# Optimization experiments

Measured on AMD Instinct MI355X. Metric: run time of the kernel, lower is better.

Reference implementation:

```python
import jax, jax.numpy as jnp
import numpy as np

NUM_HEADS = 32
HEAD_DIM = 128
HIDDEN = NUM_HEADS * HEAD_DIM  # 4096
ROPE_BASE = 10000.0
VISION_TOKEN_TYPE = 1


def vision_expert_mask(token_type_ids):
    # vision_token_mask[:, :-1] = (tt[:, :-1]==1) & (tt[:, 1:]==1); last col False
    tt = token_type_ids
    m = (tt[:, :-1] == VISION_TOKEN_TYPE) & (tt[:, 1:] == VISION_TOKEN_TYPE)
    return jnp.concatenate([m, jnp.zeros((tt.shape[0], 1), dtype=bool)], axis=1)


def rotary_cos_sin(position_ids, head_dim, dtype):
    inv_freq = 1.0 / (ROPE_BASE ** (jnp.arange(0, head_dim, 2, dtype=jnp.float32) / head_dim))
    freqs = position_ids.astype(jnp.float32)[..., None] * inv_freq  # [B,S,Dh/2]
    emb = jnp.concatenate([freqs, freqs], axis=-1)  # [B,S,Dh]
    return jnp.cos(emb).astype(dtype), jnp.sin(emb).astype(dtype)


def rotate_half(x):
    d = x.shape[-1] // 2
    return jnp.concatenate([-x[..., d:], x[..., :d]], axis=-1)


def setup_inputs() -> dict:
    key = jax.random.key(0)
    ks = jax.random.split(key, 5)
    B, S = 2, 2048
    hidden_states = jax.random.normal(ks[0], (B, S, HIDDEN), dtype=jnp.float32)
    token_type_ids = jax.random.randint(ks[1], (B, S), 0, 2, dtype=jnp.int64)
    position_ids = jnp.broadcast_to(jnp.arange(S, dtype=jnp.int64)[None, :], (B, S))
    scale = 0.02
    w_vis_qkv = jax.random.normal(ks[2], (HIDDEN, 3 * HIDDEN), dtype=jnp.float32) * scale
    w_lang_qkv = jax.random.normal(ks[3], (HIDDEN, 3 * HIDDEN), dtype=jnp.float32) * scale
    w_vis_dense = jax.random.normal(ks[4], (HIDDEN, HIDDEN), dtype=jnp.float32) * scale
    w_lang_dense = jax.random.normal(jax.random.fold_in(key, 7), (HIDDEN, HIDDEN), dtype=jnp.float32) * scale
    return dict(hidden_states=hidden_states, token_type_ids=token_type_ids,
                position_ids=position_ids, w_vis_qkv=w_vis_qkv, w_lang_qkv=w_lang_qkv,
                w_vis_dense=w_vis_dense, w_lang_dense=w_lang_dense)


def reference(hidden_states, token_type_ids, position_ids,
              w_vis_qkv, w_lang_qkv, w_vis_dense, w_lang_dense):
    B, S, D = hidden_states.shape
    vm = vision_expert_mask(token_type_ids)  # [B,S] bool

    # 2-expert QKV dispatch (mask-select between the two expert GEMMs)
    qkv = jnp.where(vm[..., None],
                    hidden_states @ w_vis_qkv,
                    hidden_states @ w_lang_qkv)  # [B,S,3D]
    q, k, v = jnp.split(qkv, 3, axis=-1)
    q = q.reshape(B, S, NUM_HEADS, HEAD_DIM)
    k = k.reshape(B, S, NUM_HEADS, HEAD_DIM)
    v = v.reshape(B, S, NUM_HEADS, HEAD_DIM)

    # rotary embedding on q, k
    cos, sin = rotary_cos_sin(position_ids, HEAD_DIM, q.dtype)  # [B,S,Dh]
    cos, sin = cos[:, :, None, :], sin[:, :, None, :]
    q = q * cos + rotate_half(q) * sin
    k = k * cos + rotate_half(k) * sin

    # causal attention (dense equivalent of the paged-attention call)
    scores = jnp.einsum('bqhd,bkhd->bhqk', q, k) / jnp.sqrt(jnp.array(HEAD_DIM, q.dtype))
    causal = jnp.tril(jnp.ones((S, S), dtype=bool))
    scores = jnp.where(causal[None, None], scores, jnp.finfo(scores.dtype).min)
    probs = jax.nn.softmax(scores, axis=-1)
    ctx = jnp.einsum('bhqk,bkhd->bqhd', probs, v).reshape(B, S, D)

    # 2-expert output dense dispatch
    attn_output = jnp.where(vm[..., None],
                            ctx @ w_vis_dense,
                            ctx @ w_lang_dense)
    return attn_output
```

## Files before the change

kernel.cpp:

```cpp
#include <hip/hip_runtime.h>
#include <math.h>

#define SEQ     2048
#define NB      2
#define NHEADS  32
#define DHEAD   128
#define HID     4096
#define NQKV    12288
#define T_TOKENS (NB*SEQ)

typedef _Float16 half8 __attribute__((ext_vector_type(8)));
typedef float v4f __attribute__((ext_vector_type(4)));

__device__ __forceinline__ void gload_lds16(const void* g, void* l) {
    __builtin_amdgcn_global_load_lds(
        (__attribute__((address_space(1))) void*)(void*)(g),
        (__attribute__((address_space(3))) void*)(unsigned)(unsigned long long)(l),
        16, 0, 0);
}

__device__ __forceinline__ v4f mfma16(half8 a, half8 b, v4f c) {
    return __builtin_amdgcn_mfma_f32_16x16x32_f16(a, b, c, 0, 0, 0);
}

__global__ void route_kernel(const int* __restrict__ tt, int* counts, int* idx) {
    int t = blockIdx.x * blockDim.x + threadIdx.x;
    if (t >= T_TOKENS) return;
    int s = t & (SEQ - 1);
    bool vm = (s < SEQ - 1) && (tt[t] == 1) && (tt[t + 1] == 1);
    int e = vm ? 0 : 1;
    int p = atomicAdd(&counts[e], 1);
    idx[e * T_TOKENS + p] = t;
}

__global__ void rope_table_kernel(const int* __restrict__ pos_ids, float2* __restrict__ tab) {
    int i = blockIdx.x * blockDim.x + threadIdx.x;
    if (i >= T_TOKENS * 64) return;
    int tok = i >> 6, j = i & 63;
    float invf = (float)pow(10000.0, -(double)j * (1.0 / 64.0));
    float ang = (float)pos_ids[tok] * invf;
    double ds, dc;
    sincos((double)ang, &ds, &dc);
    tab[i] = make_float2((float)dc, (float)ds);
}

__global__ void cvt_f32_f16(const float* __restrict__ src, _Float16* __restrict__ dst, int n4) {
    int i = blockIdx.x * blockDim.x + threadIdx.x;
    if (i >= n4) return;
    float4 v = ((const float4*)src)[i];
    union { _Float16 h[4]; uint2 u; } p;
    p.h[0] = (_Float16)v.x; p.h[1] = (_Float16)v.y;
    p.h[2] = (_Float16)v.z; p.h[3] = (_Float16)v.w;
    ((uint2*)dst)[i] = p.u;
}

__global__ void transpose_cvt(const float* __restrict__ W, _Float16* __restrict__ WT,
                              int K, int N) {
    __shared__ _Float16 t[64][72];
    const int n0 = blockIdx.x * 64, k0 = blockIdx.y * 64;
    const int cr = threadIdx.x & 15, rr = threadIdx.x >> 4;
#pragma unroll
    for (int it = 0; it < 4; ++it) {
        int r = rr + it * 16;
        float4 v = *(const float4*)&W[(size_t)(k0 + r) * N + n0 + cr * 4];
        t[cr*4+0][r] = (_Float16)v.x; t[cr*4+1][r] = (_Float16)v.y;
        t[cr*4+2][r] = (_Float16)v.z; t[cr*4+3][r] = (_Float16)v.w;
    }
    __syncthreads();
#pragma unroll
    for (int it = 0; it < 4; ++it) {
        int r = rr + it * 16;
        union { _Float16 h[4]; uint2 u; } p;
#pragma unroll
        for (int j = 0; j < 4; ++j) p.h[j] = t[r][cr*4+j];
        *(uint2*)&WT[(size_t)(n0 + r) * K + k0 + cr * 4] = p.u;
    }
}

__global__ void transpose_v(const _Float16* __restrict__ vin, _Float16* __restrict__ vout) {
    __shared__ _Float16 t[64][72];
    const int s0 = blockIdx.x * 64;
    const int d0 = blockIdx.y * 64;
    const int bh = blockIdx.z;
    const int b = bh >> 5, h = bh & 31;
    const int cr = threadIdx.x & 15, rr = threadIdx.x >> 4;
#pragma unroll
    for (int it = 0; it < 4; ++it) {
        int sl = rr + it * 16;
        union { _Float16 h4[4]; uint2 u; } p;
        p.u = *(const uint2*)&vin[(size_t)(b * SEQ + s0 + sl) * HID + h * DHEAD + d0 + cr * 4];
#pragma unroll
        for (int j = 0; j < 4; ++j) t[cr*4+j][sl] = p.h4[j];
    }
    __syncthreads();
#pragma unroll
    for (int it = 0; it < 4; ++it) {
        int dl = rr + it * 16;
        union { _Float16 h4[4]; uint2 u; } p;
#pragma unroll
        for (int j = 0; j < 4; ++j) p.h4[j] = t[dl][cr*4+j];
        *(uint2*)&vout[((size_t)bh * DHEAD + d0 + dl) * SEQ + s0 + cr * 4] = p.u;
    }
}

template <int MODE, int NCT>
__global__ __launch_bounds__(256, 2)
void gemm_expert(const _Float16* __restrict__ A,
                 const _Float16* __restrict__ BT0,
                 const _Float16* __restrict__ BT1,
                 const int* __restrict__ counts,
                 const int* __restrict__ idx_all,
                 const float2* __restrict__ rope,
                 _Float16* __restrict__ qbuf,
                 _Float16* __restrict__ kbuf,
                 _Float16* __restrict__ vbuf,
                 float* __restrict__ out) {
    const int e = blockIdx.z;
    const int count = counts[e];

    const int f   = blockIdx.x + NCT * blockIdx.y;
    const int xcd = f & 7;
    const int g   = f >> 3;
    const int c   = g >> 6;
    const int wi  = g & 63;
    const int rt  = wi >> 1;
    const int ct  = xcd * (NCT / 8) + c * 2 + (wi & 1);

    if (rt * 128 >= count) return;
    const int* idx = idx_all + e * T_TOKENS;
    const _Float16* BT = e ? BT1 : BT0;

    __shared__ _Float16 sA[4][128 * 32];
    __shared__ _Float16 sB[4][128 * 32];

    const int tid = threadIdx.x;
    const int w = tid >> 6, lane = tid & 63;
    const int col = lane & 15, quad = lane >> 4;

    const int r0 = (w * 2 + 0) * 16 + (lane >> 2);
    const int r1 = (w * 2 + 1) * 16 + (lane >> 2);
    int g0 = rt * 128 + r0; if (g0 > count - 1) g0 = count - 1;
    int g1 = rt * 128 + r1; if (g1 > count - 1) g1 = count - 1;
    const int tok0 = idx[g0], tok1 = idx[g1];
    const int schk = (lane & 3) ^ ((lane >> 3) & 3);
    const _Float16* ag0 = A + (size_t)tok0 * HID + schk * 8;
    const _Float16* ag1 = A + (size_t)tok1 * HID + schk * 8;
    const _Float16* bg0 = BT + (size_t)(ct * 128 + r0) * HID + schk * 8;
    const _Float16* bg1 = BT + (size_t)(ct * 128 + r1) * HID + schk * 8;
    const int sa_off0 = (w * 2 + 0) * 512;
    const int sa_off1 = (w * 2 + 1) * 512;

    v4f acc[2][8];
#pragma unroll
    for (int i = 0; i < 2; ++i)
#pragma unroll
        for (int j = 0; j < 8; ++j) { v4f z = {0.f, 0.f, 0.f, 0.f}; acc[i][j] = z; }

    const int kofq = (quad ^ ((col >> 1) & 3)) * 8;
    const int am0 = (w * 32 + col) * 32 + kofq;
    const int am1 = am0 + 16 * 32;

    auto stage = [&](int buf) {
        gload_lds16(ag0, &sA[buf][sa_off0]); gload_lds16(ag1, &sA[buf][sa_off1]);
        gload_lds16(bg0, &sB[buf][sa_off0]); gload_lds16(bg1, &sB[buf][sa_off1]);
        ag0 += 32; ag1 += 32; bg0 += 32; bg1 += 32;
    };
    auto compute = [&](int cur) {
        half8 a0 = *(const half8*)&sA[cur][am0];
        half8 a1 = *(const half8*)&sA[cur][am1];
#pragma unroll
        for (int nt = 0; nt < 8; ++nt) {
            half8 b = *(const half8*)&sB[cur][(nt * 16 + col) * 32 + kofq];
            acc[0][nt] = mfma16(a0, b, acc[0][nt]);
            acc[1][nt] = mfma16(a1, b, acc[1][nt]);
        }
    };

    const int NK = HID / 32;
    stage(0); stage(1); stage(2);

    for (int kt = 0; kt < NK - 3; ++kt) {
        asm volatile("s_waitcnt vmcnt(8)" ::: "memory");
        __builtin_amdgcn_s_barrier();
        asm volatile("" ::: "memory");
        stage((kt + 3) & 3);
        compute(kt & 3);
    }
    asm volatile("s_waitcnt vmcnt(8)" ::: "memory");
    __builtin_amdgcn_s_barrier();
    asm volatile("" ::: "memory");
    compute((NK - 3) & 3);
    asm volatile("s_waitcnt vmcnt(4)" ::: "memory");
    __builtin_amdgcn_s_barrier();
    asm volatile("" ::: "memory");
    compute((NK - 2) & 3);
    asm volatile("s_waitcnt vmcnt(0)" ::: "memory");
    __builtin_amdgcn_s_barrier();
    asm volatile("" ::: "memory");
    compute((NK - 1) & 3);

    const int n0 = ct * 128;
    if (MODE == 1) {
#pragma unroll
        for (int mt = 0; mt < 2; ++mt)
#pragma unroll
            for (int r = 0; r < 4; ++r) {
                int rg = rt * 128 + w * 32 + mt * 16 + quad * 4 + r;
                if (rg >= count) continue;
                int tok = idx[rg];
                float* dst = out + (size_t)tok * HID + n0;
#pragma unroll
                for (int nt = 0; nt < 8; ++nt) dst[nt * 16 + col] = acc[mt][nt][r];
            }
    } else {
        const int sec = n0 >> 12;
        const int h = (n0 >> 7) & 31;
#pragma unroll
        for (int mt = 0; mt < 2; ++mt)
#pragma unroll
            for (int r = 0; r < 4; ++r) {
                int rg = rt * 128 + w * 32 + mt * 16 + quad * 4 + r;
                if (rg >= count) continue;
                int tok = idx[rg];
                int b = tok >> 11, s = tok & (SEQ - 1);
                if (sec == 2) {
                    _Float16* dst = vbuf + (size_t)tok * HID + h * DHEAD;
#pragma unroll
                    for (int nt = 0; nt < 8; ++nt) dst[nt * 16 + col] = (_Float16)acc[mt][nt][r];
                } else {
                    _Float16* dst = (sec ? kbuf : qbuf) + ((size_t)(b * NHEADS + h) * SEQ + s) * DHEAD;
                    const float2* tp = rope + (size_t)tok * 64;
#pragma unroll
                    for (int nt = 0; nt < 4; ++nt) {
                        int d = nt * 16 + col;
                        float2 cs = tp[d];
                        float x = acc[mt][nt][r], y = acc[mt][nt + 4][r];
                        dst[d]      = (_Float16)(x * cs.x - y * cs.y);
                        dst[d + 64] = (_Float16)(y * cs.x + x * cs.y);
                    }
                }
            }
    }
}

__global__ __launch_bounds__(256, 2)
void attn_kernel(const _Float16* __restrict__ qbuf,
                 const _Float16* __restrict__ kbuf,
                 const _Float16* __restrict__ vt,
                 _Float16* __restrict__ ctx) {
    const int f   = blockIdx.x;
    const int xcd = f & 7;
    const int t   = f >> 3;
    const int s   = t & 31;
    const int rr  = t >> 5;
    const int u   = s & 15, g = s >> 4;
    const int bh  = xcd * 8 + rr * 2 + g;
    const int qt  = (rr & 1) ? (15 - u) : u;

    const int b = bh >> 5, h = bh & 31;
    const int tid = threadIdx.x;
    const int w = tid >> 6, lane = tid & 63;
    const int col = lane & 15, quad = lane >> 4;

    __shared__ _Float16 sK[2][64 * 128];
    __shared__ _Float16 sV[2][128 * 64];
    __shared__ _Float16 sP[128 * 64];

    half8 qf[2][4];
    const _Float16 qscale = (_Float16)0.08838834764831845f;
#pragma unroll
    for (int mt = 0; mt < 2; ++mt)
#pragma unroll
        for (int kc = 0; kc < 4; ++kc) {
            int row = qt * 128 + w * 32 + mt * 16 + col;
            half8 v = *(const half8*)&qbuf[((size_t)bh * SEQ + row) * DHEAD + kc * 32 + quad * 8];
            qf[mt][kc] = v * qscale;
        }

    float mrow[2][4], lrow[2][4];
    v4f o[2][8];
#pragma unroll
    for (int mt = 0; mt < 2; ++mt)
#pragma unroll
        for (int r = 0; r < 4; ++r) { mrow[mt][r] = -3.0e38f; lrow[mt][r] = 0.f; }
#pragma unroll
    for (int i = 0; i < 2; ++i)
#pragma unroll
        for (int j = 0; j < 8; ++j) { v4f z = {0.f, 0.f, 0.f, 0.f}; o[i][j] = z; }

    const int cxor = col & 7;
    const int vs_chk = (lane & 7) ^ (lane >> 3);
    const int nkt = 2 * qt + 2;

    const _Float16* kg0 = kbuf + (size_t)bh * SEQ * DHEAD;
    const _Float16* vg0 = vt + (size_t)bh * DHEAD * SEQ;

    auto stage = [&](int kt, int buf) {
        const _Float16* kg = kg0 + (size_t)kt * 64 * DHEAD;
        const _Float16* vg = vg0 + kt * 64;
#pragma unroll
        for (int op = 0; op < 4; ++op) {
            int r0 = (w * 4 + op) * 4;
            int krow = r0 + quad;
            int kcs = col ^ (krow & 7);
            gload_lds16(kg + (size_t)krow * DHEAD + kcs * 8, &sK[buf][r0 * 128]);
            int d0 = (w * 4 + op) * 8;
            int vrow = d0 + (lane >> 3);
            gload_lds16(vg + (size_t)vrow * SEQ + vs_chk * 8, &sV[buf][d0 * 64]);
        }
    };

    stage(0, 0);
    __syncthreads();

    for (int kt = 0; kt < nkt; ++kt) {
        const int cur = kt & 1;
        if (kt + 1 < nkt) stage(kt + 1, cur ^ 1);

        v4f sc[2][4];
#pragma unroll
        for (int i = 0; i < 2; ++i)
#pragma unroll
            for (int j = 0; j < 4; ++j) { v4f z = {0.f, 0.f, 0.f, 0.f}; sc[i][j] = z; }
#pragma unroll
        for (int kc = 0; kc < 4; ++kc) {
            const int kof = ((kc * 4 + quad) ^ cxor) * 8;
#pragma unroll
            for (int nt = 0; nt < 4; ++nt) {
                half8 bf = *(const half8*)&sK[cur][(size_t)(nt * 16 + col) * 128 + kof];
                sc[0][nt] = mfma16(qf[0][kc], bf, sc[0][nt]);
                sc[1][nt] = mfma16(qf[1][kc], bf, sc[1][nt]);
            }
        }

        if (kt >= 2 * qt) {
#pragma unroll
            for (int mt = 0; mt < 2; ++mt)
#pragma unroll
                for (int nt = 0; nt < 4; ++nt)
#pragma unroll
                    for (int r = 0; r < 4; ++r) {
                        int rowa = qt * 128 + w * 32 + mt * 16 + quad * 4 + r;
                        int cola = kt * 64 + nt * 16 + col;
                        if (cola > rowa) sc[mt][nt][r] = -3.0e38f;
                    }
        }

#pragma unroll
        for (int mt = 0; mt < 2; ++mt)
#pragma unroll
            for (int r = 0; r < 4; ++r) {
                float mx = sc[mt][0][r];
#pragma unroll
                for (int nt = 1; nt < 4; ++nt) mx = fmaxf(mx, sc[mt][nt][r]);
                mx = fmaxf(mx, __shfl_xor(mx, 1));
                mx = fmaxf(mx, __shfl_xor(mx, 2));
                mx = fmaxf(mx, __shfl_xor(mx, 4));
                mx = fmaxf(mx, __shfl_xor(mx, 8));
                float newm = fmaxf(mrow[mt][r], mx);
                float alpha = __expf(mrow[mt][r] - newm);
                mrow[mt][r] = newm;
                float rs = 0.f;
#pragma unroll
                for (int nt = 0; nt < 4; ++nt) {
                    float p = __expf(sc[mt][nt][r] - newm);
                    sc[mt][nt][r] = p;
                    rs += p;
                }
                rs += __shfl_xor(rs, 1); rs += __shfl_xor(rs, 2);
                rs += __shfl_xor(rs, 4); rs += __shfl_xor(rs, 8);
                lrow[mt][r] = lrow[mt][r] * alpha + rs;
#pragma unroll
                for (int nt = 0; nt < 8; ++nt) o[mt][nt][r] *= alpha;
            }

#pragma unroll
        for (int mt = 0; mt < 2; ++mt)
#pragma unroll
            for (int nt = 0; nt < 4; ++nt)
#pragma unroll
                for (int r = 0; r < 4; ++r) {
                    int rp = w * 32 + mt * 16 + quad * 4 + r;
                    int colh = nt * 16 + col;
                    int c = (colh >> 3) ^ (rp & 7);
                    sP[(size_t)rp * 64 + c * 8 + (colh & 7)] = (_Float16)sc[mt][nt][r];
                }

#pragma unroll
        for (int kc = 0; kc < 2; ++kc) {
            const int kof = ((kc * 4 + quad) ^ cxor) * 8;
            half8 p0 = *(const half8*)&sP[(size_t)(w * 32 + col) * 64 + kof];
            half8 p1 = *(const half8*)&sP[(size_t)(w * 32 + 16 + col) * 64 + kof];
#pragma unroll
            for (int nt = 0; nt < 8; ++nt) {
                half8 vf = *(const half8*)&sV[cur][(size_t)(nt * 16 + col) * 64 + kof];
                o[0][nt] = mfma16(p0, vf, o[0][nt]);
                o[1][nt] = mfma16(p1, vf, o[1][nt]);
            }
        }

        __syncthreads();
    }

#pragma unroll
    for (int mt = 0; mt < 2; ++mt)
#pragma unroll
        for (int r = 0; r < 4; ++r) {
            int rowa = qt * 128 + w * 32 + mt * 16 + quad * 4 + r;
            float inv = 1.0f / lrow[mt][r];
            _Float16* dst = ctx + ((size_t)b * SEQ + rowa) * HID + h * DHEAD;
#pragma unroll
            for (int nt = 0; nt < 8; ++nt)
                dst[nt * 16 + col] = (_Float16)(o[mt][nt][r] * inv);
        }
}

extern "C" void kernel_launch(void* const* d_in, const int* in_sizes, int n_in,
                              void* d_out, int out_size, void* d_ws, size_t ws_size,
                              hipStream_t stream) {
    const float* hidden = (const float*)d_in[0];
    const int*   tt     = (const int*)d_in[1];
    const int*   pos    = (const int*)d_in[2];
    const float* wvq    = (const float*)d_in[3];
    const float* wlq    = (const float*)d_in[4];
    const float* wvd    = (const float*)d_in[5];
    const float* wld    = (const float*)d_in[6];
    float* out = (float*)d_out;

    char* ws = (char*)d_ws;
    size_t off = 0;
    auto alloc = [&](size_t bytes) {
        char* p = ws + off;
        off += (bytes + 255) & ~(size_t)255;
        return p;
    };
    const size_t TOKB = (size_t)T_TOKENS * HID * sizeof(_Float16);
    _Float16* h16  = (_Float16*)alloc(TOKB);
    _Float16* wvqT = (_Float16*)alloc((size_t)NQKV * HID * 2);
    _Float16* wlqT = (_Float16*)alloc((size_t)NQKV * HID * 2);
    _Float16* wvdT = (_Float16*)alloc((size_t)HID * HID * 2);
    _Float16* wldT = (_Float16*)alloc((size_t)HID * HID * 2);
    _Float16* qb   = (_Float16*)alloc(TOKB);
    _Float16* kb   = (_Float16*)alloc(TOKB);
    _Float16* vtmp = (_Float16*)alloc(TOKB);
    int* counts = (int*)alloc(2 * sizeof(int));
    int* idx    = (int*)alloc(2 * T_TOKENS * sizeof(int));
    float2* rope = (float2*)alloc((size_t)T_TOKENS * 64 * sizeof(float2));
    _Float16* vT  = h16;
    _Float16* ctx = vtmp;

    hipMemsetAsync(counts, 0, 2 * sizeof(int), stream);
    route_kernel<<<T_TOKENS / 256, 256, 0, stream>>>(tt, counts, idx);
    rope_table_kernel<<<(T_TOKENS * 64) / 256, 256, 0, stream>>>(pos, rope);
    cvt_f32_f16<<<(T_TOKENS * HID / 4) / 256, 256, 0, stream>>>(hidden, h16, T_TOKENS * HID / 4);
    transpose_cvt<<<dim3(NQKV / 64, HID / 64), 256, 0, stream>>>(wvq, wvqT, HID, NQKV);
    transpose_cvt<<<dim3(NQKV / 64, HID / 64), 256, 0, stream>>>(wlq, wlqT, HID, NQKV);
    transpose_cvt<<<dim3(HID / 64, HID / 64), 256, 0, stream>>>(wvd, wvdT, HID, HID);
    transpose_cvt<<<dim3(HID / 64, HID / 64), 256, 0, stream>>>(wld, wldT, HID, HID);
    gemm_expert<0, NQKV / 128><<<dim3(NQKV / 128, T_TOKENS / 128, 2), 256, 0, stream>>>(
        h16, wvqT, wlqT, counts, idx, rope, qb, kb, vtmp, nullptr);
    transpose_v<<<dim3(SEQ / 64, DHEAD / 64, NB * NHEADS), 256, 0, stream>>>(vtmp, vT);
    attn_kernel<<<dim3(16 * NB * NHEADS), 256, 0, stream>>>(qb, kb, vT, ctx);
    gemm_expert<1, HID / 128><<<dim3(HID / 128, T_TOKENS / 128, 2), 256, 0, stream>>>(
        ctx, wvdT, wldT, counts, idx, nullptr, nullptr, nullptr, nullptr, out);
}
```

Measured before the change: 1.520 ms.

## Reshape expert GEMM wave tiles to 64x64 and trade pipeline depth for occupancy

Each wave in the expert GEMM now computes a 64x64 sub-tile in a 2x2 wave grid instead of a 32x128 strip. This lowers LDS fragment loads per MFMA (8 loads per 16 MFMAs instead of 10). The LDS ring drops from four stages to three with a matching vmcnt schedule, and launch bounds rise to three blocks per CU so more blocks can overlap. The epilogue and RoPE pairing are remapped to the interleaved column tiles. The shallower prefetch could expose more global-load latency, and the tighter register budget could cause spills.

```diff
diff --git a/kernel.cpp b/kernel.cpp
--- a/kernel.cpp
+++ b/kernel.cpp
@@ -104,7 +104,7 @@
 }
 
 template <int MODE, int NCT>
-__global__ __launch_bounds__(256, 2)
+__global__ __launch_bounds__(256, 3)
 void gemm_expert(const _Float16* __restrict__ A,
                  const _Float16* __restrict__ BT0,
                  const _Float16* __restrict__ BT1,
@@ -130,12 +130,13 @@
     const int* idx = idx_all + e * T_TOKENS;
     const _Float16* BT = e ? BT1 : BT0;
 
-    __shared__ _Float16 sA[4][128 * 32];
-    __shared__ _Float16 sB[4][128 * 32];
+    __shared__ _Float16 sA[3][128 * 32];
+    __shared__ _Float16 sB[3][128 * 32];
 
     const int tid = threadIdx.x;
     const int w = tid >> 6, lane = tid & 63;
     const int col = lane & 15, quad = lane >> 4;
+    const int wm = w >> 1, wn = w & 1;
 
     const int r0 = (w * 2 + 0) * 16 + (lane >> 2);
     const int r1 = (w * 2 + 1) * 16 + (lane >> 2);
@@ -150,15 +151,13 @@
     const int sa_off0 = (w * 2 + 0) * 512;
     const int sa_off1 = (w * 2 + 1) * 512;
 
-    v4f acc[2][8];
-#pragma unroll
-    for (int i = 0; i < 2; ++i)
-#pragma unroll
-        for (int j = 0; j < 8; ++j) { v4f z = {0.f, 0.f, 0.f, 0.f}; acc[i][j] = z; }
+    v4f acc[4][4];
+#pragma unroll
+    for (int i = 0; i < 4; ++i)
+#pragma unroll
+        for (int j = 0; j < 4; ++j) { v4f z = {0.f, 0.f, 0.f, 0.f}; acc[i][j] = z; }
 
     const int kofq = (quad ^ ((col >> 1) & 3)) * 8;
-    const int am0 = (w * 32 + col) * 32 + kofq;
-    const int am1 = am0 + 16 * 32;
 
     auto stage = [&](int buf) {
         gload_lds16(ag0, &sA[buf][sa_off0]); gload_lds16(ag1, &sA[buf][sa_off1]);
@@ -166,75 +165,79 @@
         ag0 += 32; ag1 += 32; bg0 += 32; bg1 += 32;
     };
     auto compute = [&](int cur) {
-        half8 a0 = *(const half8*)&sA[cur][am0];
-        half8 a1 = *(const half8*)&sA[cur][am1];
-#pragma unroll
-        for (int nt = 0; nt < 8; ++nt) {
-            half8 b = *(const half8*)&sB[cur][(nt * 16 + col) * 32 + kofq];
-            acc[0][nt] = mfma16(a0, b, acc[0][nt]);
-            acc[1][nt] = mfma16(a1, b, acc[1][nt]);
-        }
+        half8 a[4], b[4];
+#pragma unroll
+        for (int i = 0; i < 4; ++i)
+            a[i] = *(const half8*)&sA[cur][(wm * 64 + i * 16 + col) * 32 + kofq];
+#pragma unroll
+        for (int j = 0; j < 4; ++j)
+            b[j] = *(const half8*)&sB[cur][((wn + 2 * j) * 16 + col) * 32 + kofq];
+#pragma unroll
+        for (int i = 0; i < 4; ++i)
+#pragma unroll
+            for (int j = 0; j < 4; ++j)
+                acc[i][j] = mfma16(a[i], b[j], acc[i][j]);
     };
 
     const int NK = HID / 32;
-    stage(0); stage(1); stage(2);
-
-    for (int kt = 0; kt < NK - 3; ++kt) {
-        asm volatile("s_waitcnt vmcnt(8)" ::: "memory");
+    stage(0); stage(1);
+
+    int cur = 0, nxt = 2;
+    for (int kt = 0; kt < NK - 2; ++kt) {
+        asm volatile("s_waitcnt vmcnt(4)" ::: "memory");
         __builtin_amdgcn_s_barrier();
         asm volatile("" ::: "memory");
-        stage((kt + 3) & 3);
-        compute(kt & 3);
-    }
-    asm volatile("s_waitcnt vmcnt(8)" ::: "memory");
-    __builtin_amdgcn_s_barrier();
-    asm volatile("" ::: "memory");
-    compute((NK - 3) & 3);
+        stage(nxt);
+        compute(cur);
+        cur = (cur == 2) ? 0 : cur + 1;
+        nxt = (nxt == 2) ? 0 : nxt + 1;
+    }
     asm volatile("s_waitcnt vmcnt(4)" ::: "memory");
     __builtin_amdgcn_s_barrier();
     asm volatile("" ::: "memory");
-    compute((NK - 2) & 3);
+    compute(cur);
+    cur = (cur == 2) ? 0 : cur + 1;
     asm volatile("s_waitcnt vmcnt(0)" ::: "memory");
     __builtin_amdgcn_s_barrier();
     asm volatile("" ::: "memory");
-    compute((NK - 1) & 3);
+    compute(cur);
 
     const int n0 = ct * 128;
     if (MODE == 1) {
 #pragma unroll
-        for (int mt = 0; mt < 2; ++mt)
+        for (int i = 0; i < 4; ++i)
 #pragma unroll
             for (int r = 0; r < 4; ++r) {
-                int rg = rt * 128 + w * 32 + mt * 16 + quad * 4 + r;
+                int rg = rt * 128 + wm * 64 + i * 16 + quad * 4 + r;
                 if (rg >= count) continue;
                 int tok = idx[rg];
                 float* dst = out + (size_t)tok * HID + n0;
 #pragma unroll
-                for (int nt = 0; nt < 8; ++nt) dst[nt * 16 + col] = acc[mt][nt][r];
+                for (int j = 0; j < 4; ++j) dst[(wn + 2 * j) * 16 + col] = acc[i][j][r];
             }
     } else {
         const int sec = n0 >> 12;
         const int h = (n0 >> 7) & 31;
 #pragma unroll
-        for (int mt = 0; mt < 2; ++mt)
+        for (int i = 0; i < 4; ++i)
 #pragma unroll
             for (int r = 0; r < 4; ++r) {
-                int rg = rt * 128 + w * 32 + mt * 16 + quad * 4 + r;
+                int rg = rt * 128 + wm * 64 + i * 16 + quad * 4 + r;
                 if (rg >= count) continue;
                 int tok = idx[rg];
                 int b = tok >> 11, s = tok & (SEQ - 1);
                 if (sec == 2) {
                     _Float16* dst = vbuf + (size_t)tok * HID + h * DHEAD;
 #pragma unroll
-                    for (int nt = 0; nt < 8; ++nt) dst[nt * 16 + col] = (_Float16)acc[mt][nt][r];
+                    for (int j = 0; j < 4; ++j) dst[(wn + 2 * j) * 16 + col] = (_Float16)acc[i][j][r];
                 } else {
                     _Float16* dst = (sec ? kbuf : qbuf) + ((size_t)(b * NHEADS + h) * SEQ + s) * DHEAD;
                     const float2* tp = rope + (size_t)tok * 64;
 #pragma unroll
-                    for (int nt = 0; nt < 4; ++nt) {
-                        int d = nt * 16 + col;
+                    for (int j = 0; j < 2; ++j) {
+                        int d = (wn + 2 * j) * 16 + col;
                         float2 cs = tp[d];
-                        float x = acc[mt][nt][r], y = acc[mt][nt + 4][r];
+                        float x = acc[i][j][r], y = acc[i][j + 2][r];
                         dst[d]      = (_Float16)(x * cs.x - y * cs.y);
                         dst[d + 64] = (_Float16)(y * cs.x + x * cs.y);
                     }
```

Result: no change. 1.549 ms (+1.9%).
